# Kernel optimization log

Measured on AMD Instinct MI355X. Metric: run time of the kernel, lower is better.

Reference implementation:

```python
import jax, jax.numpy as jnp
import numpy as np

B, N, DIM = 4, 2048, 512
HEADS, DIM_HEAD = 8, 64
HID = HEADS * DIM_HEAD


def setup_inputs() -> dict:
    key = jax.random.key(0)
    k1, k2, k3, k4, k5 = jax.random.split(key, 5)
    x = jax.random.normal(k1, (B, N, DIM), jnp.float32)
    pos_bias = jax.random.normal(k2, (HEADS, N, N), jnp.float32) * 0.02
    focus_present_mask = jax.random.bernoulli(k3, 0.5, (B,))
    w_qkv = jax.random.normal(k4, (DIM, 3 * HID), jnp.float32) * (DIM ** -0.5)
    w_out = jax.random.normal(k5, (HID, DIM), jnp.float32) * (HID ** -0.5)
    return {"x": x, "pos_bias": pos_bias, "focus_present_mask": focus_present_mask,
            "w_qkv": w_qkv, "w_out": w_out}


def reference(x, pos_bias, focus_present_mask, w_qkv, w_out):
    scale = DIM_HEAD ** -0.5
    qkv = x @ w_qkv                                   # (B, N, 3*HID)
    q, k, v = jnp.split(qkv, 3, axis=-1)

    def to_heads(t):  # (B, N, HID) -> (B, H, N, D)
        return t.reshape(B, N, HEADS, DIM_HEAD).transpose(0, 2, 1, 3)

    q = to_heads(q) * scale
    k = to_heads(k)
    v = to_heads(v)

    sim = jnp.einsum('bhid,bhjd->bhij', q, k) + pos_bias[None]  # (B, H, N, N)

    # focus_present_mask[b] True -> attend only to self (eye); False -> attend all
    eye = jnp.eye(N, dtype=bool)
    mask = jnp.where(focus_present_mask[:, None, None, None],
                     eye[None, None], jnp.bool_(True))          # (B,1,N,N)
    sim = jnp.where(mask, sim, -jnp.finfo(sim.dtype).max)

    attn = jax.nn.softmax(sim, axis=-1)  # stable softmax == subtract-max + softmax
    out = jnp.einsum('bhij,bhjd->bhid', attn, v)
    out = out.transpose(0, 2, 1, 3).reshape(B, N, HID)
    return out @ w_out
```

## Files before the change

kernel.cpp:

```cpp
#include <hip/hip_runtime.h>
#include <hip/hip_bf16.h>
#include <float.h>

#define B_   4
#define N_   2048
#define DIM_ 512
#define H_   8
#define DH_  64

typedef unsigned short ushort;
typedef __attribute__((ext_vector_type(8))) short short8;
typedef __attribute__((ext_vector_type(4))) float f32x4;

__device__ __forceinline__ ushort f2bf(float f) {
    union { float f; unsigned u; } v; v.f = f;
    return (ushort)((v.u + 0x7fffu + ((v.u >> 16) & 1u)) >> 16);
}
__device__ __forceinline__ float bf2f(ushort u) {
    union { unsigned u; float f; } v; v.u = ((unsigned)u) << 16;
    return v.f;
}

typedef const __attribute__((address_space(1))) unsigned int* gas_t;
typedef __attribute__((address_space(3))) unsigned int* las_t;
__device__ __forceinline__ void gl_lds16(const void* g, void* l) {
    __builtin_amdgcn_global_load_lds((gas_t)g, (las_t)l, 16, 0, 0);
}

__global__ __launch_bounds__(256) void prep_kernel(
    const float* __restrict__ x, const float* __restrict__ wqkv,
    const float* __restrict__ wo,
    ushort* __restrict__ xb, ushort* __restrict__ wqkvT, ushort* __restrict__ woT)
{
    __shared__ ushort tile[64][72];
    const int bx = blockIdx.x;
    const int t = threadIdx.x;
    if (bx < 2048) {
        int gid = bx * 256 + t;
        const float4* xv = (const float4*)x;
        float4 v0 = xv[gid * 2], v1 = xv[gid * 2 + 1];
        uint4 pk;
        pk.x = (unsigned)f2bf(v0.x) | ((unsigned)f2bf(v0.y) << 16);
        pk.y = (unsigned)f2bf(v0.z) | ((unsigned)f2bf(v0.w) << 16);
        pk.z = (unsigned)f2bf(v1.x) | ((unsigned)f2bf(v1.y) << 16);
        pk.w = (unsigned)f2bf(v1.z) | ((unsigned)f2bf(v1.w) << 16);
        ((uint4*)xb)[gid] = pk;
        return;
    }
    int bi = bx - 2048;
    const float* src; ushort* dst; int C, tc, tr;
    if (bi < 192) { src = wqkv; dst = wqkvT; C = 1536; tc = bi % 24; tr = bi / 24; }
    else { bi -= 192; src = wo; dst = woT; C = 512; tc = bi & 7; tr = bi >> 3; }

    const int row = t >> 2, c16 = (t & 3) * 16;
    const float* sp = src + (size_t)(tr * 64 + row) * C + tc * 64 + c16;
    #pragma unroll
    for (int i = 0; i < 4; ++i) {
        float4 v = ((const float4*)sp)[i];
        tile[row][c16 + i * 4 + 0] = f2bf(v.x);
        tile[row][c16 + i * 4 + 1] = f2bf(v.y);
        tile[row][c16 + i * 4 + 2] = f2bf(v.z);
        tile[row][c16 + i * 4 + 3] = f2bf(v.w);
    }
    __syncthreads();
    ushort s[16];
    #pragma unroll
    for (int i = 0; i < 16; ++i) s[i] = tile[c16 + i][row];
    ushort* dp = dst + (size_t)(tc * 64 + row) * 512 + tr * 64 + c16;
    *(uint4*)dp       = *(uint4*)&s[0];
    *(uint4*)(dp + 8) = *(uint4*)&s[8];
}

__global__ __launch_bounds__(256) void vtrans_kernel(
    const ushort* __restrict__ v, ushort* __restrict__ vT)
{
    __shared__ ushort tile[64][72];
    const int nt = blockIdx.x, bh = blockIdx.y;
    const int t = threadIdx.x;
    const int row = t >> 2, c16 = (t & 3) * 16;
    const ushort* src = v + ((size_t)bh * 2048 + nt * 64 + row) * 64 + c16;
    *(uint4*)&tile[row][c16]     = *(const uint4*)src;
    *(uint4*)&tile[row][c16 + 8] = *(const uint4*)(src + 8);
    __syncthreads();
    ushort s[16];
    #pragma unroll
    for (int i = 0; i < 16; ++i) s[i] = tile[c16 + i][row];
    ushort* dst = vT + ((size_t)bh * 64 + row) * 2048 + nt * 64 + c16;
    *(uint4*)dst       = *(uint4*)&s[0];
    *(uint4*)(dst + 8) = *(uint4*)&s[8];
}

__global__ __launch_bounds__(256) void qkv_gemm(
    const ushort* __restrict__ A, const ushort* __restrict__ Bt,
    ushort* __restrict__ qb, ushort* __restrict__ kb, ushort* __restrict__ vb)
{
    __shared__ ushort sA[128 * 64];
    __shared__ ushort sB[128 * 64];
    const int bn = blockIdx.x;
    const int bm = blockIdx.y;
    const int t = threadIdx.x, w_id = t >> 6, lane = t & 63;
    const int l15 = lane & 15, quad = lane >> 4;
    const int mo = (w_id & 1) * 64, no = (w_id >> 1) * 64;
    const int lr = lane >> 3, lc = (lane & 7) * 8;

    f32x4 acc[4][4] = {};

    for (int kt = 0; kt < 8; ++kt) {
        __syncthreads();
        #pragma unroll
        for (int i = 0; i < 4; ++i) {
            int j = w_id * 4 + i;
            gl_lds16(A  + (size_t)(bm * 128 + j * 8 + lr) * 512 + kt * 64 + lc, &sA[j * 512]);
            gl_lds16(Bt + (size_t)(bn * 128 + j * 8 + lr) * 512 + kt * 64 + lc, &sB[j * 512]);
        }
        __syncthreads();
        #pragma unroll
        for (int c = 0; c < 2; ++c) {
            short8 af[4], bf[4];
            #pragma unroll
            for (int mt = 0; mt < 4; ++mt)
                af[mt] = *(const short8*)&sA[(mo + mt * 16 + l15) * 64 + c * 32 + quad * 8];
            #pragma unroll
            for (int n2 = 0; n2 < 4; ++n2)
                bf[n2] = *(const short8*)&sB[(no + n2 * 16 + l15) * 64 + c * 32 + quad * 8];
            #pragma unroll
            for (int mt = 0; mt < 4; ++mt)
                #pragma unroll
                for (int n2 = 0; n2 < 4; ++n2)
                    acc[mt][n2] = __builtin_amdgcn_mfma_f32_16x16x32_bf16(af[mt], bf[n2], acc[mt][n2], 0, 0, 0);
        }
    }

    const int gn0 = bn * 128 + no;
    const int which = gn0 >> 9;
    const int h = (gn0 >> 6) & 7;
    ushort* dst = which == 0 ? qb : (which == 1 ? kb : vb);
    const float sc = which == 0 ? 0.125f : 1.0f;
    #pragma unroll
    for (int mt = 0; mt < 4; ++mt) {
        const int m0 = bm * 128 + mo + mt * 16 + quad * 4;
        #pragma unroll
        for (int n2 = 0; n2 < 4; ++n2) {
            int d = n2 * 16 + l15;
            #pragma unroll
            for (int r = 0; r < 4; ++r) {
                int m = m0 + r, b = m >> 11, n = m & 2047;
                dst[((size_t)(b * 8 + h) * 2048 + n) * 64 + d] = f2bf(acc[mt][n2][r] * sc);
            }
        }
    }
}

__global__ __launch_bounds__(256) void attn_kernel(
    const ushort* __restrict__ qg, const ushort* __restrict__ kg,
    const ushort* __restrict__ vTg, const float* __restrict__ bias,
    const int* __restrict__ mask,
    ushort* __restrict__ po, float* __restrict__ pl)
{
    const int bid = blockIdx.x;
    const int qblk = bid & 31, s = (bid >> 5) & 1, h = (bid >> 6) & 7, b = bid >> 9;
    if (mask[b] != 0) return;

    const int t = threadIdx.x, w_id = t >> 6, lane = t & 63;
    const int l15 = lane & 15, quad = lane >> 4;
    const int lr = lane >> 3, lc = (lane & 7) * 8;
    const int bh = b * 8 + h;
    const int kbase = s * 1024;

    __shared__ ushort lds_k[64 * 64];
    __shared__ ushort lds_vt[64 * 64];
    __shared__ ushort lds_sp[4 * 16 * 68];

    const ushort* kptr = kg  + (size_t)bh * 2048 * 64;
    const ushort* vtp  = vTg + (size_t)bh * 64 * 2048;

    const ushort* qrp = qg + (size_t)bh * 2048 * 64 + (size_t)(qblk * 64 + w_id * 16 + l15) * 64;
    short8 qf0 = *(const short8*)(qrp + quad * 8);
    short8 qf1 = *(const short8*)(qrp + 32 + quad * 8);

    const int qrow0 = qblk * 64 + w_id * 16 + quad * 4;
    const float* bp = bias + ((size_t)h * 2048 + qrow0) * 2048 + kbase;

    float breg[16];
    #pragma unroll
    for (int tt = 0; tt < 4; ++tt)
        #pragma unroll
        for (int r = 0; r < 4; ++r)
            breg[tt * 4 + r] = bp[(size_t)r * 2048 + tt * 16 + l15];

    f32x4 o[4] = {};
    float lsum[4] = {0.f, 0.f, 0.f, 0.f};

    for (int it = 0; it < 16; ++it) {
        __syncthreads();
        #pragma unroll
        for (int i = 0; i < 2; ++i) {
            int j = w_id * 2 + i;
            gl_lds16(kptr + (size_t)(kbase + it * 64 + j * 8 + lr) * 64 + lc, &lds_k[j * 512]);
            gl_lds16(vtp + (size_t)(j * 8 + lr) * 2048 + kbase + it * 64 + lc, &lds_vt[j * 512]);
        }
        __syncthreads();

        f32x4 sv[4] = {};
        #pragma unroll
        for (int tt = 0; tt < 4; ++tt) {
            short8 kf0 = *(const short8*)&lds_k[(tt * 16 + l15) * 64 + quad * 8];
            short8 kf1 = *(const short8*)&lds_k[(tt * 16 + l15) * 64 + 32 + quad * 8];
            sv[tt] = __builtin_amdgcn_mfma_f32_16x16x32_bf16(qf0, kf0, sv[tt], 0, 0, 0);
            sv[tt] = __builtin_amdgcn_mfma_f32_16x16x32_bf16(qf1, kf1, sv[tt], 0, 0, 0);
        }
        #pragma unroll
        for (int tt = 0; tt < 4; ++tt)
            #pragma unroll
            for (int r = 0; r < 4; ++r)
                sv[tt][r] += breg[tt * 4 + r];

        if (it < 15) {
            #pragma unroll
            for (int tt = 0; tt < 4; ++tt)
                #pragma unroll
                for (int r = 0; r < 4; ++r)
                    breg[tt * 4 + r] = bp[(size_t)r * 2048 + (it + 1) * 64 + tt * 16 + l15];
        }

        const int prow0 = (w_id * 16 + quad * 4) * 68;
        #pragma unroll
        for (int r = 0; r < 4; ++r) {
            float e0 = __expf(sv[0][r]), e1 = __expf(sv[1][r]);
            float e2 = __expf(sv[2][r]), e3 = __expf(sv[3][r]);
            lsum[r] += (e0 + e1) + (e2 + e3);
            const int pr = prow0 + r * 68;
            lds_sp[pr + l15]      = f2bf(e0);
            lds_sp[pr + 16 + l15] = f2bf(e1);
            lds_sp[pr + 32 + l15] = f2bf(e2);
            lds_sp[pr + 48 + l15] = f2bf(e3);
        }

        asm volatile("s_waitcnt lgkmcnt(0)" ::: "memory");

        short8 pf0 = *(const short8*)&lds_sp[(w_id * 16 + l15) * 68 + quad * 8];
        short8 pf1 = *(const short8*)&lds_sp[(w_id * 16 + l15) * 68 + 32 + quad * 8];
        #pragma unroll
        for (int nt = 0; nt < 4; ++nt) {
            short8 vf0 = *(const short8*)&lds_vt[(nt * 16 + l15) * 64 + quad * 8];
            short8 vf1 = *(const short8*)&lds_vt[(nt * 16 + l15) * 64 + 32 + quad * 8];
            o[nt] = __builtin_amdgcn_mfma_f32_16x16x32_bf16(pf0, vf0, o[nt], 0, 0, 0);
            o[nt] = __builtin_amdgcn_mfma_f32_16x16x32_bf16(pf1, vf1, o[nt], 0, 0, 0);
        }
    }

    #pragma unroll
    for (int r = 0; r < 4; ++r) {
        #pragma unroll
        for (int off = 1; off < 16; off <<= 1)
            lsum[r] += __shfl_xor(lsum[r], off, 64);
    }

    #pragma unroll
    for (int r = 0; r < 4; ++r) {
        const int qrow = qrow0 + r;
        const size_t base = ((size_t)(s * 32 + bh) * 2048 + qrow) * 64;
        #pragma unroll
        for (int nt = 0; nt < 4; ++nt)
            po[base + nt * 16 + l15] = f2bf(o[nt][r]);
        if (l15 == 0)
            pl[(size_t)(s * 32 + bh) * 2048 + qrow] = lsum[r];
    }
}

__global__ __launch_bounds__(256) void combine_kernel(
    const ushort* __restrict__ po, const float* __restrict__ pl,
    const ushort* __restrict__ vb, const int* __restrict__ mask,
    ushort* __restrict__ ob)
{
    const int gid = blockIdx.x * 256 + threadIdx.x;
    const int dd = (gid & 7) * 8;
    const int h = (gid >> 3) & 7, n = (gid >> 6) & 2047, b = gid >> 17;
    const int bh = b * 8 + h;
    ushort* op = ob + ((size_t)b * 2048 + n) * 512 + h * 64 + dd;
    if (mask[b] != 0) {
        *(uint4*)op = *(const uint4*)(vb + ((size_t)bh * 2048 + n) * 64 + dd);
        return;
    }
    const size_t i1 = (size_t)bh * 2048 + n;
    const size_t i2 = (size_t)(32 + bh) * 2048 + n;
    float inv = 1.f / (pl[i1] + pl[i2]);
    uint4 ua = *(const uint4*)(po + i1 * 64 + dd);
    uint4 ub = *(const uint4*)(po + i2 * 64 + dd);
    const ushort* pa = (const ushort*)&ua;
    const ushort* pb = (const ushort*)&ub;
    ushort res[8];
    #pragma unroll
    for (int j = 0; j < 8; ++j)
        res[j] = f2bf((bf2f(pa[j]) + bf2f(pb[j])) * inv);
    *(uint4*)op = *(uint4*)res;
}

__global__ __launch_bounds__(256) void out_gemm(
    const ushort* __restrict__ A, const ushort* __restrict__ Bt,
    float* __restrict__ out)
{
    __shared__ ushort sA[128 * 64];
    __shared__ ushort sB[128 * 64];
    const int bn = blockIdx.x;
    const int bm = blockIdx.y;
    const int t = threadIdx.x, w_id = t >> 6, lane = t & 63;
    const int l15 = lane & 15, quad = lane >> 4;
    const int mo = (w_id & 1) * 64, no = (w_id >> 1) * 64;
    const int lr = lane >> 3, lc = (lane & 7) * 8;

    f32x4 acc[4][4] = {};

    for (int kt = 0; kt < 8; ++kt) {
        __syncthreads();
        #pragma unroll
        for (int i = 0; i < 4; ++i) {
            int j = w_id * 4 + i;
            gl_lds16(A  + (size_t)(bm * 128 + j * 8 + lr) * 512 + kt * 64 + lc, &sA[j * 512]);
            gl_lds16(Bt + (size_t)(bn * 128 + j * 8 + lr) * 512 + kt * 64 + lc, &sB[j * 512]);
        }
        __syncthreads();
        #pragma unroll
        for (int c = 0; c < 2; ++c) {
            short8 af[4], bf[4];
            #pragma unroll
            for (int mt = 0; mt < 4; ++mt)
                af[mt] = *(const short8*)&sA[(mo + mt * 16 + l15) * 64 + c * 32 + quad * 8];
            #pragma unroll
            for (int n2 = 0; n2 < 4; ++n2)
                bf[n2] = *(const short8*)&sB[(no + n2 * 16 + l15) * 64 + c * 32 + quad * 8];
            #pragma unroll
            for (int mt = 0; mt < 4; ++mt)
                #pragma unroll
                for (int n2 = 0; n2 < 4; ++n2)
                    acc[mt][n2] = __builtin_amdgcn_mfma_f32_16x16x32_bf16(af[mt], bf[n2], acc[mt][n2], 0, 0, 0);
        }
    }
    #pragma unroll
    for (int mt = 0; mt < 4; ++mt) {
        const int m0 = bm * 128 + mo + mt * 16 + quad * 4;
        #pragma unroll
        for (int n2 = 0; n2 < 4; ++n2) {
            int col = bn * 128 + no + n2 * 16 + l15;
            #pragma unroll
            for (int r = 0; r < 4; ++r)
                out[(size_t)(m0 + r) * 512 + col] = acc[mt][n2][r];
        }
    }
}

extern "C" void kernel_launch(void* const* d_in, const int* in_sizes, int n_in,
                              void* d_out, int out_size, void* d_ws, size_t ws_size,
                              hipStream_t stream)
{
    const float* x        = (const float*)d_in[0];
    const float* pos_bias = (const float*)d_in[1];
    const int*   mask     = (const int*)d_in[2];
    const float* w_qkv    = (const float*)d_in[3];
    const float* w_out    = (const float*)d_in[4];
    float* out = (float*)d_out;

    char* ws = (char*)d_ws;
    ushort* qb    = (ushort*)(ws + 0);
    ushort* kb    = (ushort*)(ws + 8388608);
    ushort* vb    = (ushort*)(ws + 16777216);
    ushort* vT    = (ushort*)(ws + 25165824);
    ushort* xb    = (ushort*)(ws + 33554432);
    ushort* ob    = (ushort*)(ws + 33554432);
    ushort* po    = (ushort*)(ws + 41943040);
    float*  pl    = (float* )(ws + 58720256);
    ushort* woT   = (ushort*)(ws + 59244544);
    ushort* wqkvT = (ushort*)(ws + 59768832);

    prep_kernel<<<2304, 256, 0, stream>>>(x, w_qkv, w_out, xb, wqkvT, woT);
    qkv_gemm<<<dim3(12, 64), 256, 0, stream>>>(xb, wqkvT, qb, kb, vb);
    vtrans_kernel<<<dim3(32, 32), 256, 0, stream>>>(vb, vT);
    attn_kernel<<<2048, 256, 0, stream>>>(qb, kb, vT, pos_bias, mask, po, pl);
    combine_kernel<<<2048, 256, 0, stream>>>(po, pl, vb, mask, ob);
    out_gemm<<<dim3(4, 64), 256, 0, stream>>>(ob, woT, out);
}
```

Before: 299.3 us.

## Fuse V transpose into QKV GEMM, skip masked Q/K tiles, double-buffer out GEMM

The QKV GEMM epilogue now also writes the transposed V layout directly, which removes the separate vtrans kernel launch and its extra read/write pass. QKV blocks that produce Q or K for batches whose focus mask is set exit early, because attention for those batches only needs V. The output GEMM gains double-buffered LDS with prefetch of the next K tile and an XOR swizzle to reduce bank conflicts. The tradeoffs are doubled LDS use in out_gemm, which may lower occupancy, and scattered 8-byte stores for vT.

```diff
diff --git a/kernel.cpp b/kernel.cpp
--- a/kernel.cpp
+++ b/kernel.cpp
@@ -71,33 +71,18 @@
     *(uint4*)(dp + 8) = *(uint4*)&s[8];
 }
 
-__global__ __launch_bounds__(256) void vtrans_kernel(
-    const ushort* __restrict__ v, ushort* __restrict__ vT)
-{
-    __shared__ ushort tile[64][72];
-    const int nt = blockIdx.x, bh = blockIdx.y;
-    const int t = threadIdx.x;
-    const int row = t >> 2, c16 = (t & 3) * 16;
-    const ushort* src = v + ((size_t)bh * 2048 + nt * 64 + row) * 64 + c16;
-    *(uint4*)&tile[row][c16]     = *(const uint4*)src;
-    *(uint4*)&tile[row][c16 + 8] = *(const uint4*)(src + 8);
-    __syncthreads();
-    ushort s[16];
-    #pragma unroll
-    for (int i = 0; i < 16; ++i) s[i] = tile[c16 + i][row];
-    ushort* dst = vT + ((size_t)bh * 64 + row) * 2048 + nt * 64 + c16;
-    *(uint4*)dst       = *(uint4*)&s[0];
-    *(uint4*)(dst + 8) = *(uint4*)&s[8];
-}
-
 __global__ __launch_bounds__(256) void qkv_gemm(
     const ushort* __restrict__ A, const ushort* __restrict__ Bt,
-    ushort* __restrict__ qb, ushort* __restrict__ kb, ushort* __restrict__ vb)
+    const int* __restrict__ mask,
+    ushort* __restrict__ qb, ushort* __restrict__ kb, ushort* __restrict__ vb,
+    ushort* __restrict__ vT)
 {
     __shared__ ushort sA[128 * 64];
     __shared__ ushort sB[128 * 64];
     const int bn = blockIdx.x;
     const int bm = blockIdx.y;
+    if (bn < 8 && mask[bm >> 4] != 0) return;
+
     const int t = threadIdx.x, w_id = t >> 6, lane = t & 63;
     const int l15 = lane & 15, quad = lane >> 4;
     const int mo = (w_id & 1) * 64, no = (w_id >> 1) * 64;
@@ -142,10 +127,21 @@
         #pragma unroll
         for (int n2 = 0; n2 < 4; ++n2) {
             int d = n2 * 16 + l15;
+            ushort w0, w1, w2, w3;
             #pragma unroll
             for (int r = 0; r < 4; ++r) {
                 int m = m0 + r, b = m >> 11, n = m & 2047;
-                dst[((size_t)(b * 8 + h) * 2048 + n) * 64 + d] = f2bf(acc[mt][n2][r] * sc);
+                ushort bfv = f2bf(acc[mt][n2][r] * sc);
+                dst[((size_t)(b * 8 + h) * 2048 + n) * 64 + d] = bfv;
+                if (r == 0) w0 = bfv; else if (r == 1) w1 = bfv;
+                else if (r == 2) w2 = bfv; else w3 = bfv;
+            }
+            if (which == 2) {
+                int b = m0 >> 11, n0 = m0 & 2047;
+                uint2 pk;
+                pk.x = (unsigned)w0 | ((unsigned)w1 << 16);
+                pk.y = (unsigned)w2 | ((unsigned)w3 << 16);
+                *(uint2*)&vT[((size_t)(b * 8 + h) * 64 + d) * 2048 + n0] = pk;
             }
         }
     }
@@ -300,41 +296,57 @@
     const ushort* __restrict__ A, const ushort* __restrict__ Bt,
     float* __restrict__ out)
 {
-    __shared__ ushort sA[128 * 64];
-    __shared__ ushort sB[128 * 64];
+    __shared__ ushort sA[2][128 * 64];
+    __shared__ ushort sB[2][128 * 64];
     const int bn = blockIdx.x;
     const int bm = blockIdx.y;
     const int t = threadIdx.x, w_id = t >> 6, lane = t & 63;
     const int l15 = lane & 15, quad = lane >> 4;
     const int mo = (w_id & 1) * 64, no = (w_id >> 1) * 64;
-    const int lr = lane >> 3, lc = (lane & 7) * 8;
+    const int lr = lane >> 3;
+    const int lcs = ((lane & 7) ^ lr) * 8;
+    const int rsw = l15 & 7;
 
     f32x4 acc[4][4] = {};
 
+    #pragma unroll
+    for (int i = 0; i < 4; ++i) {
+        int j = w_id * 4 + i;
+        gl_lds16(A  + (size_t)(bm * 128 + j * 8 + lr) * 512 + lcs, &sA[0][j * 512]);
+        gl_lds16(Bt + (size_t)(bn * 128 + j * 8 + lr) * 512 + lcs, &sB[0][j * 512]);
+    }
+    asm volatile("s_waitcnt vmcnt(0)" ::: "memory");
+    __syncthreads();
+
     for (int kt = 0; kt < 8; ++kt) {
-        __syncthreads();
-        #pragma unroll
-        for (int i = 0; i < 4; ++i) {
-            int j = w_id * 4 + i;
-            gl_lds16(A  + (size_t)(bm * 128 + j * 8 + lr) * 512 + kt * 64 + lc, &sA[j * 512]);
-            gl_lds16(Bt + (size_t)(bn * 128 + j * 8 + lr) * 512 + kt * 64 + lc, &sB[j * 512]);
-        }
-        __syncthreads();
+        const int cur = kt & 1;
+        if (kt + 1 < 8) {
+            #pragma unroll
+            for (int i = 0; i < 4; ++i) {
+                int j = w_id * 4 + i;
+                gl_lds16(A  + (size_t)(bm * 128 + j * 8 + lr) * 512 + (kt + 1) * 64 + lcs,
+                         &sA[cur ^ 1][j * 512]);
+                gl_lds16(Bt + (size_t)(bn * 128 + j * 8 + lr) * 512 + (kt + 1) * 64 + lcs,
+                         &sB[cur ^ 1][j * 512]);
+            }
+        }
         #pragma unroll
         for (int c = 0; c < 2; ++c) {
             short8 af[4], bf[4];
             #pragma unroll
             for (int mt = 0; mt < 4; ++mt)
-                af[mt] = *(const short8*)&sA[(mo + mt * 16 + l15) * 64 + c * 32 + quad * 8];
+                af[mt] = *(const short8*)&sA[cur][(mo + mt * 16 + l15) * 64 + (((c * 4 + quad) ^ rsw)) * 8];
             #pragma unroll
             for (int n2 = 0; n2 < 4; ++n2)
-                bf[n2] = *(const short8*)&sB[(no + n2 * 16 + l15) * 64 + c * 32 + quad * 8];
+                bf[n2] = *(const short8*)&sB[cur][(no + n2 * 16 + l15) * 64 + (((c * 4 + quad) ^ rsw)) * 8];
             #pragma unroll
             for (int mt = 0; mt < 4; ++mt)
                 #pragma unroll
                 for (int n2 = 0; n2 < 4; ++n2)
                     acc[mt][n2] = __builtin_amdgcn_mfma_f32_16x16x32_bf16(af[mt], bf[n2], acc[mt][n2], 0, 0, 0);
         }
+        asm volatile("s_waitcnt vmcnt(0)" ::: "memory");
+        __syncthreads();
     }
     #pragma unroll
     for (int mt = 0; mt < 4; ++mt) {
@@ -373,8 +385,7 @@
     ushort* wqkvT = (ushort*)(ws + 59768832);
 
     prep_kernel<<<2304, 256, 0, stream>>>(x, w_qkv, w_out, xb, wqkvT, woT);
-    qkv_gemm<<<dim3(12, 64), 256, 0, stream>>>(xb, wqkvT, qb, kb, vb);
-    vtrans_kernel<<<dim3(32, 32), 256, 0, stream>>>(vb, vT);
+    qkv_gemm<<<dim3(12, 64), 256, 0, stream>>>(xb, wqkvT, mask, qb, kb, vb, vT);
     attn_kernel<<<2048, 256, 0, stream>>>(qb, kb, vT, pos_bias, mask, po, pl);
     combine_kernel<<<2048, 256, 0, stream>>>(po, pl, vb, mask, ob);
     out_gemm<<<dim3(4, 64), 256, 0, stream>>>(ob, woT, out);
```

Result: faster. 292.2 us (-2.4%).
